# Optimization experiments

Hardware: AMD Instinct MI355X
Metric: run time of the kernel (lower is better)

Reference implementation:

```python
import jax, jax.numpy as jnp
import numpy as np
import math

N_NODES = 50000
N_EDGES = 640000
IN_FEATS = 128
HEADS = 8
OUT_FEATS = 16
D_FF = 4 * IN_FEATS


def setup_inputs() -> dict:
    key = jax.random.key(0)
    ks = jax.random.split(key, 10)
    s = 0.05
    return {
        "feat": jax.random.normal(ks[0], (N_NODES, IN_FEATS), jnp.float32),
        "src": jax.random.randint(ks[1], (N_EDGES,), 0, N_NODES, jnp.int32),
        "dst": jax.random.randint(ks[2], (N_EDGES,), 0, N_NODES, jnp.int32),
        "Wq": jax.random.normal(ks[3], (IN_FEATS, HEADS * OUT_FEATS), jnp.float32) * s,
        "Wk": jax.random.normal(ks[4], (IN_FEATS, HEADS * OUT_FEATS), jnp.float32) * s,
        "Wv": jax.random.normal(ks[5], (IN_FEATS, HEADS * OUT_FEATS), jnp.float32) * s,
        "ln1_g": jnp.ones((IN_FEATS,), jnp.float32),
        "ln1_b": jnp.zeros((IN_FEATS,), jnp.float32),
        "W1": jax.random.normal(ks[6], (IN_FEATS, D_FF), jnp.float32) * s,
        "b1": jnp.zeros((D_FF,), jnp.float32),
        "prelu_a": jnp.full((D_FF,), 0.25, jnp.float32),  # torch PReLU default init
        "W2": jax.random.normal(ks[7], (D_FF, IN_FEATS), jnp.float32) * s,
        "b2": jnp.zeros((IN_FEATS,), jnp.float32),
    }


def layer_norm(x, g, b, eps=1e-5):
    mu = jnp.mean(x, axis=-1, keepdims=True)
    var = jnp.mean(jnp.square(x - mu), axis=-1, keepdims=True)
    return (x - mu) * jax.lax.rsqrt(var + eps) * g + b


def reference(feat, src, dst, Wq, Wk, Wv, ln1_g, ln1_b, W1, b1, prelu_a, W2, b2):
    N = feat.shape[0]
    feat_c = jax.lax.stop_gradient(feat)  # feat.clone().detach()
    q = (feat @ Wq).reshape(N, HEADS, OUT_FEATS)
    k = (feat_c @ Wk).reshape(N, HEADS, OUT_FEATS)
    v = (feat_c @ Wv).reshape(N, HEADS, OUT_FEATS)

    # edge score: dot(k[src], q[dst]) per head -> [E, H]
    e = jnp.einsum('ehd,ehd->eh', k[src], q[dst]) / math.sqrt(OUT_FEATS * HEADS)

    # segment softmax over incoming edges of each dst node
    m = jax.ops.segment_max(e, dst, num_segments=N)          # [N, H]
    e_exp = jnp.exp(e - m[dst])                              # [E, H]
    denom = jax.ops.segment_sum(e_exp, dst, num_segments=N)  # [N, H]
    a = e_exp / denom[dst]                                   # [E, H]

    # weighted scatter-sum aggregation
    msg = v[src] * a[:, :, None]                             # [E, H, D]
    ft2 = jax.ops.segment_sum(msg, dst, num_segments=N)      # [N, H, D]

    rst = ft2.reshape(feat.shape) + feat
    # NOTE: original applies ln1 twice (ln2 is unused) -- reproduced faithfully
    rst = layer_norm(rst, ln1_g, ln1_b)
    h = rst @ W1 + b1
    h = jnp.where(h >= 0, h, prelu_a * h)                    # PReLU, per-channel
    ffn = h @ W2 + b2
    rst = layer_norm(rst + ffn, ln1_g, ln1_b)
    return rst
```

## Files before the change

### kernel.cpp

```cpp
#include <hip/hip_runtime.h>

#define N_NODES 50000
#define N_EDGES 640000
#define F 128
#define DFF 512
#define NB 196

using u32 = unsigned int;
using u16 = unsigned short;

typedef __bf16 bf16x8 __attribute__((ext_vector_type(8)));
typedef float f32x4 __attribute__((ext_vector_type(4)));

__device__ __forceinline__ float bf2f(u16 u) {
    return __uint_as_float(((u32)u) << 16);
}
__device__ __forceinline__ float blo(u32 p) { return __uint_as_float(p << 16); }
__device__ __forceinline__ float bhi(u32 p) { return __uint_as_float(p & 0xffff0000u); }
__device__ __forceinline__ u16 f2bf(float f) {
    u32 u = __float_as_uint(f);
    u += 0x7fffu + ((u >> 16) & 1u);
    return (u16)(u >> 16);
}
__device__ __forceinline__ u32 pack2(float a, float b) {
    return (u32)f2bf(a) | ((u32)f2bf(b) << 16);
}

#define FEAT_UNITS (N_NODES * F / 4)
#define PH_TOTAL (FEAT_UNITS + 180224 + N_EDGES)
__global__ void k_prep(const float* __restrict__ feat, u16* __restrict__ featb,
                       const float* __restrict__ Wq, const float* __restrict__ Wk,
                       const float* __restrict__ Wv, const float* __restrict__ W1,
                       const float* __restrict__ W2, u16* __restrict__ WT,
                       const int* __restrict__ dst, int* __restrict__ cnt) {
    int idx = blockIdx.x * 256 + threadIdx.x;
    if (idx < FEAT_UNITS) {
        float4 v = reinterpret_cast<const float4*>(feat)[idx];
        uint2 p;
        p.x = pack2(v.x, v.y);
        p.y = pack2(v.z, v.w);
        reinterpret_cast<uint2*>(featb)[idx] = p;
        return;
    }
    int wi = idx - FEAT_UNITS;
    if (wi < 180224) {
        if (wi < 49152) {
            int mi = wi >> 14;
            int local = wi & 16383;
            const float* W = (mi == 0) ? Wq : ((mi == 1) ? Wk : Wv);
            int n = local >> 7, k = local & 127;
            WT[wi] = f2bf(W[(size_t)k * 128 + n]);
        } else if (wi < 114688) {
            int local = wi - 49152;
            int n = local >> 7, k = local & 127;
            WT[wi] = f2bf(W1[(size_t)k * 512 + n]);
        } else {
            int local = wi - 114688;
            int n = local >> 9, k = local & 511;
            WT[wi] = f2bf(W2[(size_t)k * 128 + n]);
        }
        return;
    }
    int e = wi - 180224;
    if (e < N_EDGES) atomicAdd(&cnt[dst[e]], 1);
}

__global__ void k_bsum(const int* __restrict__ counts, int* __restrict__ bsum) {
    int i = blockIdx.x * 256 + threadIdx.x;
    int v = (i < N_NODES) ? counts[i] : 0;
#pragma unroll
    for (int off = 32; off >= 1; off >>= 1) v += __shfl_xor(v, off, 64);
    __shared__ int ws[4];
    int lane = threadIdx.x & 63, wid = threadIdx.x >> 6;
    if (lane == 0) ws[wid] = v;
    __syncthreads();
    if (threadIdx.x == 0) bsum[blockIdx.x] = ws[0] + ws[1] + ws[2] + ws[3];
}

__global__ void k_bfill(const int* __restrict__ counts, const int* __restrict__ bsum,
                        int* __restrict__ row_ptr) {
    int b = blockIdx.x, t = threadIdx.x;
    int lane = t & 63, wid = t >> 6;
    __shared__ int ws[4];
    __shared__ int sboff[256];

    int bv = (t < NB) ? bsum[t] : 0;
    int bincl = bv;
#pragma unroll
    for (int off = 1; off < 64; off <<= 1) {
        int u = __shfl_up(bincl, off, 64);
        if (lane >= off) bincl += u;
    }
    if (lane == 63) ws[wid] = bincl;
    __syncthreads();
    int bwo = 0;
#pragma unroll
    for (int j = 0; j < 4; ++j) if (j < wid) bwo += ws[j];
    sboff[t] = bwo + bincl - bv;
    __syncthreads();
    const int boff = sboff[b];

    int i = b * 256 + t;
    int v = (i < N_NODES) ? counts[i] : 0;
    int incl = v;
#pragma unroll
    for (int off = 1; off < 64; off <<= 1) {
        int u = __shfl_up(incl, off, 64);
        if (lane >= off) incl += u;
    }
    if (lane == 63) ws[wid] = incl;
    __syncthreads();
    int wo = 0;
#pragma unroll
    for (int j = 0; j < 4; ++j) if (j < wid) wo += ws[j];
    if (i < N_NODES) row_ptr[i] = boff + wo + incl - v;
    if (i == 0) row_ptr[N_NODES] = N_EDGES;
}

__global__ void k_fill(const int* __restrict__ src, const int* __restrict__ dst,
                       const int* __restrict__ row_ptr, int* __restrict__ fill,
                       int* __restrict__ csr_src) {
    int e = blockIdx.x * 256 + threadIdx.x;
    if (e < N_EDGES) {
        int d = dst[e];
        int pos = row_ptr[d] + atomicAdd(&fill[d], 1);
        csr_src[pos] = src[e];
    }
}

template <int EPI>
__global__ __launch_bounds__(256) void k_mm(
    const u16* __restrict__ A, int lda,
    const u16* __restrict__ BT,
    void* __restrict__ Cv, int ldc,
    int K,
    const float* __restrict__ bias,
    const float* __restrict__ prelu,
    const u16* __restrict__ resid,
    const float* __restrict__ g,
    const float* __restrict__ bb)
{
    __shared__ u16 smem[17408];
    u16* sA = smem;
    u16* sB = smem + 128 * 64;
    u16* sC = smem;

    const int t = threadIdx.x;
    const int w = t >> 6;
    const int lane = t & 63;
    const int ln = lane & 15, q4 = lane >> 4;
    const int row0 = blockIdx.x * 128;
    const int cb = blockIdx.y * 128;

    f32x4 acc[2][8];
#pragma unroll
    for (int mt = 0; mt < 2; ++mt)
#pragma unroll
        for (int nt = 0; nt < 8; ++nt)
            acc[mt][nt] = (f32x4){0.f, 0.f, 0.f, 0.f};

    uint4 pa[4], pb[4];
#define LOAD_A(kc)                                                             \
    {                                                                          \
        _Pragma("unroll") for (int i = 0; i < 4; ++i) {                        \
            int u = i * 256 + t, r = u >> 3, k8 = (u & 7) * 8;                 \
            int row = row0 + r;                                                \
            uint4 val = make_uint4(0, 0, 0, 0);                                \
            if (row < N_NODES)                                                 \
                val = *reinterpret_cast<const uint4*>(A + (size_t)row * lda + (kc) + k8); \
            pa[i] = val;                                                       \
        }                                                                      \
    }
#define LOAD_B(kc)                                                             \
    {                                                                          \
        _Pragma("unroll") for (int i = 0; i < 4; ++i) {                        \
            int u = i * 256 + t, r = u >> 3, k8 = (u & 7) * 8;                 \
            pb[i] = *reinterpret_cast<const uint4*>(BT + (size_t)(cb + r) * K + (kc) + k8); \
        }                                                                      \
    }

    LOAD_A(0);
    LOAD_B(0);

    for (int kc = 0; kc < K; kc += 64) {
#pragma unroll
        for (int i = 0; i < 4; ++i) {
            int u = i * 256 + t, r = u >> 3, gi = u & 7;
            int off = (r * 8 + (gi ^ (r & 7))) * 8;
            *reinterpret_cast<uint4*>(&sA[off]) = pa[i];
            *reinterpret_cast<uint4*>(&sB[off]) = pb[i];
        }
        __syncthreads();
        if (kc + 64 < K) {
            LOAD_A(kc + 64);
            LOAD_B(kc + 64);
        }
#pragma unroll
        for (int ks = 0; ks < 2; ++ks) {
            const int gsw = ks * 4 + q4;
            const int rA0 = w * 32 + ln;
            const int rA1 = rA0 + 16;
            bf16x8 a0 = *reinterpret_cast<const bf16x8*>(&sA[(rA0 * 8 + (gsw ^ (rA0 & 7))) * 8]);
            bf16x8 a1 = *reinterpret_cast<const bf16x8*>(&sA[(rA1 * 8 + (gsw ^ (rA1 & 7))) * 8]);
#pragma unroll
            for (int nt = 0; nt < 8; ++nt) {
                const int rB = nt * 16 + ln;
                bf16x8 b = *reinterpret_cast<const bf16x8*>(&sB[(rB * 8 + (gsw ^ (rB & 7))) * 8]);
                acc[0][nt] = __builtin_amdgcn_mfma_f32_16x16x32_bf16(a0, b, acc[0][nt], 0, 0, 0);
                acc[1][nt] = __builtin_amdgcn_mfma_f32_16x16x32_bf16(a1, b, acc[1][nt], 0, 0, 0);
            }
        }
        __syncthreads();
    }
#undef LOAD_A
#undef LOAD_B

    if (EPI == 0 || EPI == 1) {
        float bs[8], pr[8];
        if (EPI == 1) {
#pragma unroll
            for (int nt = 0; nt < 8; ++nt) {
                int col = cb + nt * 16 + ln;
                bs[nt] = bias[col];
                pr[nt] = prelu[col];
            }
        }
#pragma unroll
        for (int mt = 0; mt < 2; ++mt)
#pragma unroll
            for (int nt = 0; nt < 8; ++nt)
#pragma unroll
                for (int j = 0; j < 4; ++j) {
                    float x = acc[mt][nt][j];
                    if (EPI == 1) {
                        x += bs[nt];
                        x = (x >= 0.f) ? x : pr[nt] * x;
                    }
                    sC[(w * 32 + mt * 16 + q4 * 4 + j) * 136 + nt * 16 + ln] = f2bf(x);
                }
        __syncthreads();
        if (EPI == 0 && cb != 0) {
            u32* C32 = (u32*)Cv;
            const u32 vflag = (cb == 256) ? 1u : 0u;
#pragma unroll
            for (int i = 0; i < 8; ++i) {
                int u = i * 256 + t;
                int r = u >> 4, c8 = (u & 15) * 8;
                int row = row0 + r;
                if (row < N_NODES) {
                    const u32* srow = reinterpret_cast<const u32*>(&sC[r * 136 + c8]);
                    u32 dw = (u32)row * 192u + 64u + (u32)c8 + vflag;
                    C32[dw]     = srow[0];
                    C32[dw + 2] = srow[1];
                    C32[dw + 4] = srow[2];
                    C32[dw + 6] = srow[3];
                }
            }
        } else {
            u16* C = (u16*)Cv;
#pragma unroll
            for (int i = 0; i < 8; ++i) {
                int u = i * 256 + t;
                int r = u >> 4, c8 = (u & 15) * 8;
                int row = row0 + r;
                if (row < N_NODES) {
                    uint4 val = *reinterpret_cast<const uint4*>(&sC[r * 136 + c8]);
                    *reinterpret_cast<uint4*>(&C[(size_t)row * ldc + cb + c8]) = val;
                }
            }
        }
    } else {
        float* C = (float*)Cv;
        float bs[8], gv[8], bv[8];
#pragma unroll
        for (int nt = 0; nt < 8; ++nt) {
            int col = nt * 16 + ln;
            bs[nt] = bias[col];
            gv[nt] = g[col];
            bv[nt] = bb[col];
        }
#pragma unroll
        for (int mt = 0; mt < 2; ++mt)
#pragma unroll
            for (int j = 0; j < 4; ++j) {
                int row = row0 + w * 32 + mt * 16 + q4 * 4 + j;
                bool ok = row < N_NODES;
                float vals[8];
                float s = 0.f, ss = 0.f;
#pragma unroll
                for (int nt = 0; nt < 8; ++nt) {
                    float x = acc[mt][nt][j] + bs[nt];
                    if (ok) x += bf2f(resid[(size_t)row * 128 + nt * 16 + ln]);
                    vals[nt] = x;
                    s += x; ss += x * x;
                }
                s += __shfl_xor(s, 8, 16); ss += __shfl_xor(ss, 8, 16);
                s += __shfl_xor(s, 4, 16); ss += __shfl_xor(ss, 4, 16);
                s += __shfl_xor(s, 2, 16); ss += __shfl_xor(ss, 2, 16);
                s += __shfl_xor(s, 1, 16); ss += __shfl_xor(ss, 1, 16);
                float mu = s * (1.f / 128.f);
                float var = ss * (1.f / 128.f) - mu * mu;
                float rs = rsqrtf(var + 1e-5f);
                if (ok) {
#pragma unroll
                    for (int nt = 0; nt < 8; ++nt)
                        C[(size_t)row * 128 + nt * 16 + ln] =
                            (vals[nt] - mu) * rs * gv[nt] + bv[nt];
                }
            }
    }
}

__global__ __launch_bounds__(256) void k_attn(
    const u32* __restrict__ Q32, const float* __restrict__ feat,
    const int* __restrict__ row_ptr, const int* __restrict__ csr_src,
    const float* __restrict__ g, const float* __restrict__ bb,
    u16* __restrict__ rstb)
{
    const int w = threadIdx.x >> 6;
    const int lane = threadIdx.x & 63;
    const int n = blockIdx.x * 4 + w;
    if (n >= N_NODES) return;
    const float scale = 0.08838834764831845f;

    const u32 qp = Q32[(u32)n * 192u + (u32)lane];
    const float q0 = blo(qp), q1 = bhi(qp);
    const int e0 = row_ptr[n], e1 = row_ptr[n + 1];
    const u32 kvlane = 64u + 2u * (u32)lane;

    float l = 0.f, a0 = 0.f, a1 = 0.f;

#define LD4(S, KV)                                                                      \
    {                                                                                   \
        KV[0] = *reinterpret_cast<const uint2*>(Q32 + (u32)(S).x * 192u + kvlane);      \
        KV[1] = *reinterpret_cast<const uint2*>(Q32 + (u32)(S).y * 192u + kvlane);      \
        KV[2] = *reinterpret_cast<const uint2*>(Q32 + (u32)(S).z * 192u + kvlane);      \
        KV[3] = *reinterpret_cast<const uint2*>(Q32 + (u32)(S).w * 192u + kvlane);      \
    }
#define CG(KV)                                                                          \
    {                                                                                   \
        float p0 = blo(KV[0].x) * q0 + bhi(KV[0].x) * q1;                               \
        float p1 = blo(KV[1].x) * q0 + bhi(KV[1].x) * q1;                               \
        float p2 = blo(KV[2].x) * q0 + bhi(KV[2].x) * q1;                               \
        float p3 = blo(KV[3].x) * q0 + bhi(KV[3].x) * q1;                               \
        p0 += __shfl_xor(p0, 4, 8); p1 += __shfl_xor(p1, 4, 8);                         \
        p2 += __shfl_xor(p2, 4, 8); p3 += __shfl_xor(p3, 4, 8);                         \
        p0 += __shfl_xor(p0, 2, 8); p1 += __shfl_xor(p1, 2, 8);                         \
        p2 += __shfl_xor(p2, 2, 8); p3 += __shfl_xor(p3, 2, 8);                         \
        p0 += __shfl_xor(p0, 1, 8); p1 += __shfl_xor(p1, 1, 8);                         \
        p2 += __shfl_xor(p2, 1, 8); p3 += __shfl_xor(p3, 1, 8);                         \
        float ea = __expf(p0 * scale), eb = __expf(p1 * scale);                         \
        float ec = __expf(p2 * scale), ed = __expf(p3 * scale);                         \
        l += (ea + eb) + (ec + ed);                                                     \
        a0 += ea * blo(KV[0].y) + eb * blo(KV[1].y) + ec * blo(KV[2].y) + ed * blo(KV[3].y); \
        a1 += ea * bhi(KV[0].y) + eb * bhi(KV[1].y) + ec * bhi(KV[2].y) + ed * bhi(KV[3].y); \
    }

    int e = e0;
    int rem = e1 - e0;
    {
        int4 sA, sB;
        uint2 kvA[4], kvB[4];
        if (rem >= 4) {
            sA = *reinterpret_cast<const int4*>(csr_src + e);
            LD4(sA, kvA);
            if (rem >= 8) {
                sB = *reinterpret_cast<const int4*>(csr_src + e + 4);
                while (true) {
                    if (rem >= 12) sA = *reinterpret_cast<const int4*>(csr_src + e + 8);
                    LD4(sB, kvB);
                    CG(kvA);
                    e += 4; rem -= 4;
                    if (rem < 8) { CG(kvB); e += 4; rem -= 4; break; }
                    if (rem >= 12) sB = *reinterpret_cast<const int4*>(csr_src + e + 8);
                    LD4(sA, kvA);
                    CG(kvB);
                    e += 4; rem -= 4;
                    if (rem < 8) { CG(kvA); e += 4; rem -= 4; break; }
                }
            } else {
                CG(kvA);
                e += 4; rem -= 4;
            }
        }
    }
    for (; e < e1; ++e) {
        int s0 = csr_src[e];
        uint2 kv = *reinterpret_cast<const uint2*>(Q32 + (u32)s0 * 192u + kvlane);
        float p0 = blo(kv.x) * q0 + bhi(kv.x) * q1;
        p0 += __shfl_xor(p0, 4, 8);
        p0 += __shfl_xor(p0, 2, 8);
        p0 += __shfl_xor(p0, 1, 8);
        float ea = __expf(p0 * scale);
        l += ea;
        a0 += ea * blo(kv.y);
        a1 += ea * bhi(kv.y);
    }
#undef LD4
#undef CG

    float inv = (l > 0.f) ? 1.f / l : 0.f;
    const int c2 = lane * 2;
    const float2 fr = *reinterpret_cast<const float2*>(feat + (size_t)n * 128 + c2);
    float x0 = a0 * inv + fr.x;
    float x1 = a1 * inv + fr.y;

    float sum = x0 + x1, sq = x0 * x0 + x1 * x1;
#pragma unroll
    for (int off = 32; off >= 1; off >>= 1) {
        sum += __shfl_xor(sum, off, 64);
        sq += __shfl_xor(sq, off, 64);
    }
    float mu = sum * (1.f / 128.f);
    float var = sq * (1.f / 128.f) - mu * mu;
    float rs = rsqrtf(var + 1e-5f);
    float y0 = (x0 - mu) * rs * g[c2] + bb[c2];
    float y1 = (x1 - mu) * rs * g[c2 + 1] + bb[c2 + 1];
    reinterpret_cast<u32*>(rstb)[(size_t)n * 64 + lane] = pack2(y0, y1);
}

extern "C" void kernel_launch(void* const* d_in, const int* in_sizes, int n_in,
                              void* d_out, int out_size, void* d_ws, size_t ws_size,
                              hipStream_t stream)
{
    const float* feat = (const float*)d_in[0];
    const int* src    = (const int*)d_in[1];
    const int* dst    = (const int*)d_in[2];
    const float* Wq   = (const float*)d_in[3];
    const float* Wk   = (const float*)d_in[4];
    const float* Wv   = (const float*)d_in[5];
    const float* ln_g = (const float*)d_in[6];
    const float* ln_b = (const float*)d_in[7];
    const float* W1   = (const float*)d_in[8];
    const float* b1   = (const float*)d_in[9];
    const float* pa   = (const float*)d_in[10];
    const float* W2   = (const float*)d_in[11];
    const float* b2   = (const float*)d_in[12];

    u16* qkv   = (u16*)d_ws;
    u16* h     = qkv + (size_t)N_NODES * 384;
    u16* featb = h;
    u16* rstb  = h + (size_t)N_NODES * 512;
    u16* WT    = rstb + (size_t)N_NODES * 128;
    u16* BqkvT = WT;
    u16* W1T   = WT + 49152;
    u16* W2T   = WT + 114688;
    int* counts  = (int*)(WT + 180224);
    int* fill    = counts + N_NODES;
    int* row_ptr = fill + N_NODES;
    int* csr_src = row_ptr + N_NODES + 1;
    int* bsum    = csr_src + N_EDGES;

    hipMemsetAsync(counts, 0, sizeof(int) * 2 * N_NODES, stream);
    k_prep<<<(PH_TOTAL + 255) / 256, 256, 0, stream>>>(
        feat, featb, Wq, Wk, Wv, W1, W2, WT, dst, counts);

    k_bsum<<<NB, 256, 0, stream>>>(counts, bsum);
    k_bfill<<<NB, 256, 0, stream>>>(counts, bsum, row_ptr);
    k_fill<<<(N_EDGES + 255) / 256, 256, 0, stream>>>(src, dst, row_ptr, fill, csr_src);

    const int MBK = (N_NODES + 127) / 128;

    dim3 gqkv(MBK, 3);
    k_mm<0><<<gqkv, 256, 0, stream>>>(featb, 128, BqkvT, qkv, 384, 128,
                                      nullptr, nullptr, nullptr, nullptr, nullptr);

    k_attn<<<(N_NODES + 3) / 4, 256, 0, stream>>>((const u32*)qkv, feat, row_ptr, csr_src,
                                                  ln_g, ln_b, rstb);

    dim3 gf1(MBK, 4);
    k_mm<1><<<gf1, 256, 0, stream>>>(rstb, 128, W1T, h, 512, 128,
                                     b1, pa, nullptr, nullptr, nullptr);

    dim3 gf2(MBK, 1);
    k_mm<2><<<gf2, 256, 0, stream>>>(h, 512, W2T, d_out, 128, 512,
                                     b2, nullptr, rstb, ln_g, ln_b);
}
```

Baseline: 324.4 us.

## Store K and V in interleaved FP8 to halve attention gather bytes

The QKV projection epilogue now converts K and V outputs to FP8 (e4m3) and interleaves them per node as packed 16-bit pairs, shrinking the per-node row from 768 to 512 bytes. The attention kernel gathers one 32-bit word per lane per edge instead of a uint2 and decodes K and V with the hardware fp8 unpack instructions. This cuts the bytes fetched by the random per-edge gather, which dominates the attention kernel. In exchange, K and V lose precision, which may affect accuracy tolerance, and the epilogue now issues scattered 16-bit stores with four times as many loop iterations.

```diff
diff --git a/kernel.cpp b/kernel.cpp
--- a/kernel.cpp
+++ b/kernel.cpp
@@ -11,6 +11,7 @@
 
 typedef __bf16 bf16x8 __attribute__((ext_vector_type(8)));
 typedef float f32x4 __attribute__((ext_vector_type(4)));
+typedef float f32x2 __attribute__((ext_vector_type(2)));
 
 __device__ __forceinline__ float bf2f(u16 u) {
     return __uint_as_float(((u32)u) << 16);
@@ -240,20 +241,17 @@
                 }
         __syncthreads();
         if (EPI == 0 && cb != 0) {
-            u32* C32 = (u32*)Cv;
+            u16* C = (u16*)Cv;
             const u32 vflag = (cb == 256) ? 1u : 0u;
 #pragma unroll
-            for (int i = 0; i < 8; ++i) {
+            for (int i = 0; i < 32; ++i) {
                 int u = i * 256 + t;
-                int r = u >> 4, c8 = (u & 15) * 8;
+                int r = u >> 6, p = u & 63;
                 int row = row0 + r;
                 if (row < N_NODES) {
-                    const u32* srow = reinterpret_cast<const u32*>(&sC[r * 136 + c8]);
-                    u32 dw = (u32)row * 192u + 64u + (u32)c8 + vflag;
-                    C32[dw]     = srow[0];
-                    C32[dw + 2] = srow[1];
-                    C32[dw + 4] = srow[2];
-                    C32[dw + 6] = srow[3];
+                    u32 pair = *reinterpret_cast<const u32*>(&sC[r * 136 + p * 2]);
+                    int packed = __builtin_amdgcn_cvt_pk_fp8_f32(blo(pair), bhi(pair), 0, false);
+                    C[(u32)row * 256u + 128u + (u32)p * 2u + vflag] = (u16)(packed & 0xffff);
                 }
             }
         } else {
@@ -323,26 +321,30 @@
     if (n >= N_NODES) return;
     const float scale = 0.08838834764831845f;
 
-    const u32 qp = Q32[(u32)n * 192u + (u32)lane];
+    const u32 qp = Q32[(u32)n * 128u + (u32)lane];
     const float q0 = blo(qp), q1 = bhi(qp);
     const int e0 = row_ptr[n], e1 = row_ptr[n + 1];
-    const u32 kvlane = 64u + 2u * (u32)lane;
+    const u32 kvlane = 64u + (u32)lane;
 
     float l = 0.f, a0 = 0.f, a1 = 0.f;
 
 #define LD4(S, KV)                                                                      \
     {                                                                                   \
-        KV[0] = *reinterpret_cast<const uint2*>(Q32 + (u32)(S).x * 192u + kvlane);      \
-        KV[1] = *reinterpret_cast<const uint2*>(Q32 + (u32)(S).y * 192u + kvlane);      \
-        KV[2] = *reinterpret_cast<const uint2*>(Q32 + (u32)(S).z * 192u + kvlane);      \
-        KV[3] = *reinterpret_cast<const uint2*>(Q32 + (u32)(S).w * 192u + kvlane);      \
+        KV[0] = Q32[(u32)(S).x * 128u + kvlane];                                        \
+        KV[1] = Q32[(u32)(S).y * 128u + kvlane];                                        \
+        KV[2] = Q32[(u32)(S).z * 128u + kvlane];                                        \
+        KV[3] = Q32[(u32)(S).w * 128u + kvlane];                                        \
     }
 #define CG(KV)                                                                          \
     {                                                                                   \
-        float p0 = blo(KV[0].x) * q0 + bhi(KV[0].x) * q1;                               \
-        float p1 = blo(KV[1].x) * q0 + bhi(KV[1].x) * q1;                               \
-        float p2 = blo(KV[2].x) * q0 + bhi(KV[2].x) * q1;                               \
-        float p3 = blo(KV[3].x) * q0 + bhi(KV[3].x) * q1;                               \
+        f32x2 k0 = __builtin_amdgcn_cvt_pk_f32_fp8((int)KV[0], false);                  \
+        f32x2 k1 = __builtin_amdgcn_cvt_pk_f32_fp8((int)KV[1], false);                  \
+        f32x2 k2 = __builtin_amdgcn_cvt_pk_f32_fp8((int)KV[2], false);                  \
+        f32x2 k3 = __builtin_amdgcn_cvt_pk_f32_fp8((int)KV[3], false);                  \
+        float p0 = k0.x * q0 + k0.y * q1;                                               \
+        float p1 = k1.x * q0 + k1.y * q1;                                               \
+        float p2 = k2.x * q0 + k2.y * q1;                                               \
+        float p3 = k3.x * q0 + k3.y * q1;                                               \
         p0 += __shfl_xor(p0, 4, 8); p1 += __shfl_xor(p1, 4, 8);                         \
         p2 += __shfl_xor(p2, 4, 8); p3 += __shfl_xor(p3, 4, 8);                         \
         p0 += __shfl_xor(p0, 2, 8); p1 += __shfl_xor(p1, 2, 8);                         \
@@ -352,15 +354,19 @@
         float ea = __expf(p0 * scale), eb = __expf(p1 * scale);                         \
         float ec = __expf(p2 * scale), ed = __expf(p3 * scale);                         \
         l += (ea + eb) + (ec + ed);                                                     \
-        a0 += ea * blo(KV[0].y) + eb * blo(KV[1].y) + ec * blo(KV[2].y) + ed * blo(KV[3].y); \
-        a1 += ea * bhi(KV[0].y) + eb * bhi(KV[1].y) + ec * bhi(KV[2].y) + ed * bhi(KV[3].y); \
+        f32x2 v0 = __builtin_amdgcn_cvt_pk_f32_fp8((int)KV[0], true);                   \
+        f32x2 v1 = __builtin_amdgcn_cvt_pk_f32_fp8((int)KV[1], true);                   \
+        f32x2 v2 = __builtin_amdgcn_cvt_pk_f32_fp8((int)KV[2], true);                   \
+        f32x2 v3 = __builtin_amdgcn_cvt_pk_f32_fp8((int)KV[3], true);                   \
+        a0 += ea * v0.x + eb * v1.x + ec * v2.x + ed * v3.x;                            \
+        a1 += ea * v0.y + eb * v1.y + ec * v2.y + ed * v3.y;                            \
     }
 
     int e = e0;
     int rem = e1 - e0;
     {
         int4 sA, sB;
-        uint2 kvA[4], kvB[4];
+        u32 kvA[4], kvB[4];
         if (rem >= 4) {
             sA = *reinterpret_cast<const int4*>(csr_src + e);
             LD4(sA, kvA);
@@ -386,15 +392,17 @@
     }
     for (; e < e1; ++e) {
         int s0 = csr_src[e];
-        uint2 kv = *reinterpret_cast<const uint2*>(Q32 + (u32)s0 * 192u + kvlane);
-        float p0 = blo(kv.x) * q0 + bhi(kv.x) * q1;
+        u32 kv = Q32[(u32)s0 * 128u + kvlane];
+        f32x2 kf = __builtin_amdgcn_cvt_pk_f32_fp8((int)kv, false);
+        float p0 = kf.x * q0 + kf.y * q1;
         p0 += __shfl_xor(p0, 4, 8);
         p0 += __shfl_xor(p0, 2, 8);
         p0 += __shfl_xor(p0, 1, 8);
         float ea = __expf(p0 * scale);
+        f32x2 vf = __builtin_amdgcn_cvt_pk_f32_fp8((int)kv, true);
         l += ea;
-        a0 += ea * blo(kv.y);
-        a1 += ea * bhi(kv.y);
+        a0 += ea * vf.x;
+        a1 += ea * vf.y;
     }
 #undef LD4
 #undef CG
@@ -462,7 +470,7 @@
     const int MBK = (N_NODES + 127) / 128;
 
     dim3 gqkv(MBK, 3);
-    k_mm<0><<<gqkv, 256, 0, stream>>>(featb, 128, BqkvT, qkv, 384, 128,
+    k_mm<0><<<gqkv, 256, 0, stream>>>(featb, 128, BqkvT, qkv, 256, 128,
                                       nullptr, nullptr, nullptr, nullptr, nullptr);
 
     k_attn<<<(N_NODES + 3) / 4, 256, 0, stream>>>((const u32*)qkv, feat, row_ptr, csr_src,
```

Result: faster. 304.2 us, median of 4 (-6.2%).
